# Performance work log

Measured on AMD Instinct MI355X. Metric: run time of the kernel, lower is better.

The kernel has to match this reference:

```python
import jax, jax.numpy as jnp
import numpy as np

N_NODES = 100000
IN_C, HID_C, OUT_C = 128, 64, 40
N_EDGES = 1600000


def setup_inputs() -> dict:
    key = jax.random.key(0)
    k1, k2, k3, k4, k5, k6 = jax.random.split(key, 6)
    x = jax.random.normal(k1, (N_NODES, IN_C), dtype=jnp.float32)
    edge_index = jax.random.randint(k2, (2, N_EDGES), 0, N_NODES, dtype=jnp.int32)
    # Glorot-style init for GCN weights, zero bias (as in PyG GCNConv)
    W1 = jax.random.normal(k3, (IN_C, HID_C), dtype=jnp.float32) / np.sqrt(IN_C)
    b1 = jnp.zeros((HID_C,), dtype=jnp.float32)
    W2 = jax.random.normal(k4, (HID_C, OUT_C), dtype=jnp.float32) / np.sqrt(HID_C)
    b2 = jnp.zeros((OUT_C,), dtype=jnp.float32)
    return {"x": x, "edge_index": edge_index, "W1": W1, "b1": b1, "W2": W2, "b2": b2}


def gcn_conv(x, src, dst, W, b, n_nodes):
    # PyG GCNConv: self-loops added, symmetric deg^{-1/2} normalization,
    # linear transform first, then normalized scatter-sum aggregation, then bias.
    deg = jnp.zeros((n_nodes,), dtype=x.dtype).at[dst].add(1.0)
    dinv = jnp.where(deg > 0, jax.lax.rsqrt(deg), 0.0)
    norm = dinv[src] * dinv[dst]                      # [E]
    h = x @ W                                          # [N, out]
    msg = h[src] * norm[:, None]                       # [E, out] (gather)
    out = jax.ops.segment_sum(msg, dst, num_segments=n_nodes)  # scatter-add
    return out + b


def reference(x, edge_index, W1, b1, W2, b2):
    n = x.shape[0]
    loop = jnp.arange(n, dtype=edge_index.dtype)
    src = jnp.concatenate([edge_index[0], loop])
    dst = jnp.concatenate([edge_index[1], loop])
    h = jax.nn.relu(gcn_conv(x, src, dst, W1, b1, n))
    # F.dropout with training=False -> identity (eval mode)
    return gcn_conv(h, src, dst, W2, b2, n)
```

## Files before the change

### kernel.cpp

```cpp
#include <hip/hip_runtime.h>

#define N_NODES 100000
#define IN_C    128
#define HID_C   64
#define OUT_C   40
#define N_EDGES 1600000

#define BSH        8
#define NBUCK      ((N_NODES + 255) >> BSH)
#define CAP        5120
#define PART_CHUNK 4096
#define NPB        ((N_EDGES + PART_CHUNK - 1) / PART_CHUNK)
#define EPT        (PART_CHUNK / 256)

typedef _Float16 half_t;
typedef _Float16 half8   __attribute__((ext_vector_type(8)));
typedef _Float16 half2_t __attribute__((ext_vector_type(2)));
typedef float    f32x4   __attribute__((ext_vector_type(4)));
typedef unsigned long long ull;

static __device__ __forceinline__ void acc8(float* a, uint2 v, float sc) {
    char4 lo = __builtin_bit_cast(char4, v.x);
    char4 hi = __builtin_bit_cast(char4, v.y);
    a[0] += sc * (float)lo.x; a[1] += sc * (float)lo.y;
    a[2] += sc * (float)lo.z; a[3] += sc * (float)lo.w;
    a[4] += sc * (float)hi.x; a[5] += sc * (float)hi.y;
    a[6] += sc * (float)hi.z; a[7] += sc * (float)hi.w;
}

static __device__ __forceinline__ void acc_q(float4& a, unsigned v, float sc, bool ok) {
    char4 c = __builtin_bit_cast(char4, v);
    if (ok) {
        a.x += sc * (float)c.x;
        a.y += sc * (float)c.y;
        a.z += sc * (float)c.z;
        a.w += sc * (float)c.w;
    }
}

__global__ void k_init(const float* __restrict__ W1, const float* __restrict__ W2,
                       half_t* __restrict__ W1T, half_t* __restrict__ W2T,
                       int* __restrict__ gcur) {
    int t = threadIdx.x;
    if (t < NBUCK) gcur[t] = t * CAP;
    for (int i = t; i < IN_C * HID_C; i += 512) {
        int k = i >> 6, n = i & 63;
        W1T[n * IN_C + k] = (half_t)W1[i];
    }
    for (int i = t; i < 48 * HID_C; i += 512) {
        int n = i >> 6, k = i & 63;
        W2T[n * HID_C + k] = (n < OUT_C) ? (half_t)W2[k * OUT_C + n] : (half_t)0.0f;
    }
}

__global__ void k_part(const int* __restrict__ src, const int* __restrict__ dst,
                       int* __restrict__ gcur, ull* __restrict__ pairs) {
    __shared__ int lh[NBUCK];
    int tid = threadIdx.x;
    for (int i = tid; i < NBUCK; i += 256) lh[i] = 0;
    __syncthreads();
    int base = blockIdx.x * PART_CHUNK;
    int sv[EPT], dv[EPT], rv[EPT];
#pragma unroll
    for (int j = 0; j < EPT; ++j) {
        int e = base + j * 256 + tid;
        if (e < N_EDGES) {
            sv[j] = src[e];
            dv[j] = dst[e];
            rv[j] = atomicAdd(&lh[dv[j] >> BSH], 1);
        } else {
            dv[j] = -1;
        }
    }
    __syncthreads();
    for (int i = tid; i < NBUCK; i += 256) {
        int c = lh[i];
        if (c) lh[i] = atomicAdd(&gcur[i], c);
    }
    __syncthreads();
#pragma unroll
    for (int j = 0; j < EPT; ++j) {
        if (dv[j] >= 0) {
            int pos = lh[dv[j] >> BSH] + rv[j];
            pairs[pos] = ((ull)(unsigned)dv[j] << 32) | (unsigned)sv[j];
        }
    }
}

__global__ void k_bbuild(const ull* __restrict__ pairs, const int* __restrict__ gcur,
                         int* __restrict__ cursor, int* __restrict__ cnt,
                         float* __restrict__ dinv, int* __restrict__ esrc) {
    __shared__ int lc[256];
    __shared__ int ls[256];
    __shared__ int lcur[256];
    int b = blockIdx.x, tid = threadIdx.x;
    int nbase = b << BSH;
    int s0 = b * CAP, s1 = gcur[b];

    lc[tid] = 0;
    __syncthreads();
    for (int e = s0 + tid; e < s1; e += 256)
        atomicAdd(&lc[(int)(pairs[e] >> 32) - nbase], 1);
    __syncthreads();

    int v = lc[tid];
    ls[tid] = v;
    __syncthreads();
    for (int off = 1; off < 256; off <<= 1) {
        int t = (tid >= off) ? ls[tid - off] : 0;
        __syncthreads();
        ls[tid] += t;
        __syncthreads();
    }
    int excl = ls[tid] - v;
    int node = nbase + tid;
    int rowstart = s0 + excl;
    lcur[tid] = rowstart;
    if (node < N_NODES) {
        cursor[node] = rowstart;
        cnt[node]    = v;
        dinv[node]   = rsqrtf(1.0f + (float)v);
    }
    __syncthreads();

    for (int e = s0 + tid; e < s1; e += 256) {
        ull p = pairs[e];
        int d = (int)(p >> 32);
        int s = (int)(p & 0xffffffffu);
        int pos = atomicAdd(&lcur[d - nbase], 1);
        esrc[pos] = s;
    }
}

__global__ void k_gemm1_mfma(const float* __restrict__ x, const half_t* __restrict__ W1T,
                             const float* __restrict__ dinv, signed char* __restrict__ g1q,
                             float* __restrict__ scales) {
    __shared__ __align__(16) signed char lq[16 * HID_C];
    int lane = threadIdx.x & 63;
    int l16  = lane & 15;
    int lg   = lane >> 4;

    half8 bf[4][4];
#pragma unroll
    for (int ct = 0; ct < 4; ++ct)
#pragma unroll
        for (int kc = 0; kc < 4; ++kc)
            bf[ct][kc] = *(const half8*)(W1T + (ct * 16 + l16) * IN_C + kc * 32 + lg * 8);

#pragma unroll
    for (int s = 0; s < 2; ++s) {
        int r0 = (blockIdx.x * 2 + s) * 16;
        f32x4 acc0 = {0.f, 0.f, 0.f, 0.f};
        f32x4 acc1 = {0.f, 0.f, 0.f, 0.f};
        f32x4 acc2 = {0.f, 0.f, 0.f, 0.f};
        f32x4 acc3 = {0.f, 0.f, 0.f, 0.f};
#pragma unroll
        for (int kc = 0; kc < 4; ++kc) {
            const float* ap = x + (size_t)(r0 + l16) * IN_C + kc * 32 + lg * 8;
            float4 a0 = *(const float4*)ap;
            float4 a1 = *(const float4*)(ap + 4);
            half8 af;
            af[0] = (_Float16)a0.x; af[1] = (_Float16)a0.y;
            af[2] = (_Float16)a0.z; af[3] = (_Float16)a0.w;
            af[4] = (_Float16)a1.x; af[5] = (_Float16)a1.y;
            af[6] = (_Float16)a1.z; af[7] = (_Float16)a1.w;
            acc0 = __builtin_amdgcn_mfma_f32_16x16x32_f16(af, bf[0][kc], acc0, 0, 0, 0);
            acc1 = __builtin_amdgcn_mfma_f32_16x16x32_f16(af, bf[1][kc], acc1, 0, 0, 0);
            acc2 = __builtin_amdgcn_mfma_f32_16x16x32_f16(af, bf[2][kc], acc2, 0, 0, 0);
            acc3 = __builtin_amdgcn_mfma_f32_16x16x32_f16(af, bf[3][kc], acc3, 0, 0, 0);
        }
#pragma unroll
        for (int j = 0; j < 4; ++j) {
            int   r  = r0 + lg * 4 + j;
            float dv = dinv[r];
            float v0 = acc0[j] * dv;
            float v1 = acc1[j] * dv;
            float v2 = acc2[j] * dv;
            float v3 = acc3[j] * dv;
            float m = fmaxf(fmaxf(fabsf(v0), fabsf(v1)), fmaxf(fabsf(v2), fabsf(v3)));
            m = fmaxf(m, __shfl_xor(m, 1));
            m = fmaxf(m, __shfl_xor(m, 2));
            m = fmaxf(m, __shfl_xor(m, 4));
            m = fmaxf(m, __shfl_xor(m, 8));
            float inv = (m > 0.0f) ? 127.0f / m : 0.0f;
            if (l16 == 0) scales[r] = m * (1.0f / 127.0f);
            int q0 = min(127, max(-127, __float2int_rn(v0 * inv)));
            int q1 = min(127, max(-127, __float2int_rn(v1 * inv)));
            int q2 = min(127, max(-127, __float2int_rn(v2 * inv)));
            int q3 = min(127, max(-127, __float2int_rn(v3 * inv)));
            int rl = lg * 4 + j;
            lq[rl * HID_C +  0 + l16] = (signed char)q0;
            lq[rl * HID_C + 16 + l16] = (signed char)q1;
            lq[rl * HID_C + 32 + l16] = (signed char)q2;
            lq[rl * HID_C + 48 + l16] = (signed char)q3;
        }
        uint4 wv = *(const uint4*)(lq + lane * 16);
        *(uint4*)(g1q + (size_t)r0 * HID_C + lane * 16) = wv;
    }
}

__global__ void k_pull1(const int* __restrict__ cursor, const int* __restrict__ cnt,
                        const int* __restrict__ esrc, const float* __restrict__ dinv,
                        const uint2* __restrict__ g1v, const float* __restrict__ scales,
                        const float* __restrict__ b1, half_t* __restrict__ h1) {
    int w    = threadIdx.x >> 6;
    int lane = threadIdx.x & 63;
    int n    = blockIdx.x * 4 + w;
    int slot = lane >> 3;
    int c8   = lane & 7;

    float dn  = dinv[n];
    int start = cursor[n];
    int end   = start + cnt[n];

    float a[8] = {0.f, 0.f, 0.f, 0.f, 0.f, 0.f, 0.f, 0.f};
    if (slot == 0)
        acc8(a, g1v[(size_t)n * 8 + c8], scales[n]);

    int e = start;
    for (; e + 16 <= end; e += 16) {
        int i0 = esrc[e + slot];
        int i1 = esrc[e + 8 + slot];
        uint2 v0 = g1v[(size_t)i0 * 8 + c8];
        float s0 = scales[i0];
        uint2 v1 = g1v[(size_t)i1 * 8 + c8];
        float s1 = scales[i1];
        acc8(a, v0, s0);
        acc8(a, v1, s1);
    }
    for (; e < end; e += 8) {
        int  ee  = e + slot;
        bool ok  = ee < end;
        int  idx = esrc[ok ? ee : end - 1];
        uint2 v = g1v[(size_t)idx * 8 + c8];
        float s = ok ? scales[idx] : 0.f;
        acc8(a, v, s);
    }

#pragma unroll
    for (int j = 0; j < 8; ++j) {
        a[j] += __shfl_xor(a[j], 8);
        a[j] += __shfl_xor(a[j], 16);
        a[j] += __shfl_xor(a[j], 32);
    }

    if (slot == 0) {
        const float* bp = b1 + c8 * 8;
        float r0 = fmaxf(dn * a[0] + bp[0], 0.f);
        float r1 = fmaxf(dn * a[1] + bp[1], 0.f);
        float r2 = fmaxf(dn * a[2] + bp[2], 0.f);
        float r3 = fmaxf(dn * a[3] + bp[3], 0.f);
        float r4 = fmaxf(dn * a[4] + bp[4], 0.f);
        float r5 = fmaxf(dn * a[5] + bp[5], 0.f);
        float r6 = fmaxf(dn * a[6] + bp[6], 0.f);
        float r7 = fmaxf(dn * a[7] + bp[7], 0.f);
        half2_t p0; p0.x = (_Float16)r0; p0.y = (_Float16)r1;
        half2_t p1; p1.x = (_Float16)r2; p1.y = (_Float16)r3;
        half2_t p2; p2.x = (_Float16)r4; p2.y = (_Float16)r5;
        half2_t p3; p3.x = (_Float16)r6; p3.y = (_Float16)r7;
        uint4 u;
        u.x = __builtin_bit_cast(unsigned, p0);
        u.y = __builtin_bit_cast(unsigned, p1);
        u.z = __builtin_bit_cast(unsigned, p2);
        u.w = __builtin_bit_cast(unsigned, p3);
        *(uint4*)(h1 + (size_t)n * HID_C + c8 * 8) = u;
    }
}

__global__ void k_gemm2_mfma(const half_t* __restrict__ h1, const half_t* __restrict__ W2T,
                             const float* __restrict__ dinv, signed char* __restrict__ g2q,
                             float* __restrict__ scales2) {
    __shared__ __align__(16) signed char lq[16 * 40];
    int lane = threadIdx.x & 63;
    int l16  = lane & 15;
    int lg   = lane >> 4;

    half8 bf[3][2];
#pragma unroll
    for (int ct = 0; ct < 3; ++ct)
#pragma unroll
        for (int kc = 0; kc < 2; ++kc)
            bf[ct][kc] = *(const half8*)(W2T + (ct * 16 + l16) * HID_C + kc * 32 + lg * 8);

#pragma unroll
    for (int s = 0; s < 2; ++s) {
        int r0 = (blockIdx.x * 2 + s) * 16;
        f32x4 acc0 = {0.f, 0.f, 0.f, 0.f};
        f32x4 acc1 = {0.f, 0.f, 0.f, 0.f};
        f32x4 acc2 = {0.f, 0.f, 0.f, 0.f};
#pragma unroll
        for (int kc = 0; kc < 2; ++kc) {
            half8 af = *(const half8*)(h1 + (size_t)(r0 + l16) * HID_C + kc * 32 + lg * 8);
            acc0 = __builtin_amdgcn_mfma_f32_16x16x32_f16(af, bf[0][kc], acc0, 0, 0, 0);
            acc1 = __builtin_amdgcn_mfma_f32_16x16x32_f16(af, bf[1][kc], acc1, 0, 0, 0);
            acc2 = __builtin_amdgcn_mfma_f32_16x16x32_f16(af, bf[2][kc], acc2, 0, 0, 0);
        }
#pragma unroll
        for (int j = 0; j < 4; ++j) {
            int   r  = r0 + lg * 4 + j;
            float dv = dinv[r];
            float v0 = acc0[j] * dv;
            float v1 = acc1[j] * dv;
            float v2 = (l16 < 8) ? acc2[j] * dv : 0.0f;
            float m = fmaxf(fmaxf(fabsf(v0), fabsf(v1)), fabsf(v2));
            m = fmaxf(m, __shfl_xor(m, 1));
            m = fmaxf(m, __shfl_xor(m, 2));
            m = fmaxf(m, __shfl_xor(m, 4));
            m = fmaxf(m, __shfl_xor(m, 8));
            float inv = (m > 0.0f) ? 127.0f / m : 0.0f;
            if (l16 == 0) scales2[r] = m * (1.0f / 127.0f);
            int q0 = min(127, max(-127, __float2int_rn(v0 * inv)));
            int q1 = min(127, max(-127, __float2int_rn(v1 * inv)));
            int q2 = min(127, max(-127, __float2int_rn(v2 * inv)));
            int rl = lg * 4 + j;
            lq[rl * 40 +  0 + l16] = (signed char)q0;
            lq[rl * 40 + 16 + l16] = (signed char)q1;
            if (l16 < 8) lq[rl * 40 + 32 + l16] = (signed char)q2;
        }
        if (lane < 40)
            *(uint4*)(g2q + (size_t)r0 * 40 + lane * 16) = *(const uint4*)(lq + lane * 16);
    }
}

__global__ void k_pull2(const int* __restrict__ cursor, const int* __restrict__ cnt,
                        const int* __restrict__ esrc, const float* __restrict__ dinv,
                        const signed char* __restrict__ g2q, const float* __restrict__ scales2,
                        const float* __restrict__ b2, float* __restrict__ out) {
    int w    = threadIdx.x >> 6;
    int lane = threadIdx.x & 63;
    int n    = blockIdx.x * 4 + w;
    int slot = lane >> 3;
    int c8   = lane & 7;

    float dn  = dinv[n];
    int start = cursor[n];
    int end   = start + cnt[n];

    float a[8] = {0.f, 0.f, 0.f, 0.f, 0.f, 0.f, 0.f, 0.f};
    if (slot == 0) {
        uint2 v = *(const uint2*)(g2q + (size_t)n * 40 + c8 * 8);
        acc8(a, v, scales2[n]);
    }

    int e = start;
    for (; e + 16 <= end; e += 16) {
        int i0 = esrc[e + slot];
        int i1 = esrc[e + 8 + slot];
        uint2 v0 = *(const uint2*)(g2q + (size_t)i0 * 40 + c8 * 8);
        float s0 = scales2[i0];
        uint2 v1 = *(const uint2*)(g2q + (size_t)i1 * 40 + c8 * 8);
        float s1 = scales2[i1];
        acc8(a, v0, s0);
        acc8(a, v1, s1);
    }
    for (; e < end; e += 8) {
        int  ee  = e + slot;
        bool ok  = ee < end;
        int  idx = esrc[ok ? ee : end - 1];
        uint2 v = *(const uint2*)(g2q + (size_t)idx * 40 + c8 * 8);
        float s = ok ? scales2[idx] : 0.f;
        acc8(a, v, s);
    }

#pragma unroll
    for (int j = 0; j < 8; ++j) {
        a[j] += __shfl_xor(a[j], 8);
        a[j] += __shfl_xor(a[j], 16);
        a[j] += __shfl_xor(a[j], 32);
    }

    if (slot == 0 && c8 < 5) {
        const float* bp = b2 + c8 * 8;
        float* op = out + (size_t)n * OUT_C + c8 * 8;
        float4 r0, r1;
        r0.x = bp[0] + dn * a[0];
        r0.y = bp[1] + dn * a[1];
        r0.z = bp[2] + dn * a[2];
        r0.w = bp[3] + dn * a[3];
        r1.x = bp[4] + dn * a[4];
        r1.y = bp[5] + dn * a[5];
        r1.z = bp[6] + dn * a[6];
        r1.w = bp[7] + dn * a[7];
        *(float4*)op = r0;
        *(float4*)(op + 4) = r1;
    }
}

extern "C" void kernel_launch(void* const* d_in, const int* in_sizes, int n_in,
                              void* d_out, int out_size, void* d_ws, size_t ws_size,
                              hipStream_t stream) {
    const float* x   = (const float*)d_in[0];
    const int*   ei  = (const int*)d_in[1];
    const int*   src = ei;
    const int*   dst = ei + N_EDGES;
    const float* W1  = (const float*)d_in[2];
    const float* b1  = (const float*)d_in[3];
    const float* W2  = (const float*)d_in[4];
    const float* b2  = (const float*)d_in[5];
    float*       out = (float*)d_out;

    const int SLAB = NBUCK * CAP;
    int*    cnt    = (int*)d_ws;
    int*    cursor = cnt + N_NODES;
    int*    gcur   = cursor + N_NODES;
    half_t* w1t    = (half_t*)(gcur + NBUCK);
    half_t* w2t    = w1t + IN_C * HID_C;
    float*  dinv   = (float*)(w2t + 48 * HID_C);
    float*  scales = dinv + N_NODES;
    float*  scales2= scales + N_NODES;
    int*    esrc   = (int*)(scales2 + N_NODES);
    int*    after  = esrc + SLAB;
    ull*    pairs  = (ull*)(((uintptr_t)after + 15) & ~(uintptr_t)15);
    signed char* g1q = (signed char*)(pairs + SLAB);
    half_t* h1 = (half_t*)(g1q + (size_t)N_NODES * 64);
    signed char* g2q = (signed char*)(h1 + (size_t)N_NODES * HID_C);

    k_init<<<1, 512, 0, stream>>>(W1, W2, w1t, w2t, gcur);
    k_part<<<NPB, 256, 0, stream>>>(src, dst, gcur, pairs);
    k_bbuild<<<NBUCK, 256, 0, stream>>>(pairs, gcur, cursor, cnt, dinv, esrc);

    k_gemm1_mfma<<<N_NODES / 32, 64, 0, stream>>>(x, w1t, dinv, g1q, scales);

    k_pull1<<<N_NODES / 4, 256, 0, stream>>>(cursor, cnt, esrc, dinv,
                                             (const uint2*)g1q, scales, b1, h1);

    k_gemm2_mfma<<<N_NODES / 32, 64, 0, stream>>>(h1, w2t, dinv, g2q, scales2);

    k_pull2<<<N_NODES / 4, 256, 0, stream>>>(cursor, cnt, esrc, dinv,
                                             g2q, scales2, b2, out);
}
```

Baseline: 169.8 us.

## Split layer-1 quantized features into two column halves and aggregate each separately

```diff
diff --git a/kernel.cpp b/kernel.cpp
--- a/kernel.cpp
+++ b/kernel.cpp
@@ -133,7 +133,8 @@
 }
 
 __global__ void k_gemm1_mfma(const float* __restrict__ x, const half_t* __restrict__ W1T,
-                             const float* __restrict__ dinv, signed char* __restrict__ g1q,
+                             const float* __restrict__ dinv,
+                             signed char* __restrict__ g1qA, signed char* __restrict__ g1qB,
                              float* __restrict__ scales) {
     __shared__ __align__(16) signed char lq[16 * HID_C];
     int lane = threadIdx.x & 63;
@@ -194,76 +195,82 @@
             lq[rl * HID_C + 32 + l16] = (signed char)q2;
             lq[rl * HID_C + 48 + l16] = (signed char)q3;
         }
-        uint4 wv = *(const uint4*)(lq + lane * 16);
-        *(uint4*)(g1q + (size_t)r0 * HID_C + lane * 16) = wv;
-    }
-}
-
-__global__ void k_pull1(const int* __restrict__ cursor, const int* __restrict__ cnt,
-                        const int* __restrict__ esrc, const float* __restrict__ dinv,
-                        const uint2* __restrict__ g1v, const float* __restrict__ scales,
-                        const float* __restrict__ b1, half_t* __restrict__ h1) {
+        {
+            int row = lane >> 2;
+            int q   = lane & 3;
+            uint2 av = *(const uint2*)(lq + row * HID_C + q * 8);
+            uint2 bv = *(const uint2*)(lq + row * HID_C + 32 + q * 8);
+            *(uint2*)(g1qA + (size_t)(r0 + row) * 32 + q * 8) = av;
+            *(uint2*)(g1qB + (size_t)(r0 + row) * 32 + q * 8) = bv;
+        }
+    }
+}
+
+__global__ void k_pull1h(const int* __restrict__ cursor, const int* __restrict__ cnt,
+                         const int* __restrict__ esrc, const float* __restrict__ dinv,
+                         const unsigned* __restrict__ g1h, const float* __restrict__ scales,
+                         const float* __restrict__ b1h, half_t* __restrict__ h1h) {
     int w    = threadIdx.x >> 6;
     int lane = threadIdx.x & 63;
     int n    = blockIdx.x * 4 + w;
     int slot = lane >> 3;
-    int c8   = lane & 7;
+    int c4   = lane & 7;
 
     float dn  = dinv[n];
     int start = cursor[n];
     int end   = start + cnt[n];
 
-    float a[8] = {0.f, 0.f, 0.f, 0.f, 0.f, 0.f, 0.f, 0.f};
+    float4 acc = {0.f, 0.f, 0.f, 0.f};
     if (slot == 0)
-        acc8(a, g1v[(size_t)n * 8 + c8], scales[n]);
+        acc_q(acc, g1h[(size_t)n * 8 + c4], scales[n], true);
 
     int e = start;
-    for (; e + 16 <= end; e += 16) {
+    for (; e + 32 <= end; e += 32) {
         int i0 = esrc[e + slot];
         int i1 = esrc[e + 8 + slot];
-        uint2 v0 = g1v[(size_t)i0 * 8 + c8];
-        float s0 = scales[i0];
-        uint2 v1 = g1v[(size_t)i1 * 8 + c8];
-        float s1 = scales[i1];
-        acc8(a, v0, s0);
-        acc8(a, v1, s1);
+        int i2 = esrc[e + 16 + slot];
+        int i3 = esrc[e + 24 + slot];
+        unsigned v0 = g1h[(size_t)i0 * 8 + c4];
+        float    s0 = scales[i0];
+        unsigned v1 = g1h[(size_t)i1 * 8 + c4];
+        float    s1 = scales[i1];
+        unsigned v2 = g1h[(size_t)i2 * 8 + c4];
+        float    s2 = scales[i2];
+        unsigned v3 = g1h[(size_t)i3 * 8 + c4];
+        float    s3 = scales[i3];
+        acc_q(acc, v0, s0, true);
+        acc_q(acc, v1, s1, true);
+        acc_q(acc, v2, s2, true);
+        acc_q(acc, v3, s3, true);
     }
     for (; e < end; e += 8) {
         int  ee  = e + slot;
         bool ok  = ee < end;
         int  idx = esrc[ok ? ee : end - 1];
-        uint2 v = g1v[(size_t)idx * 8 + c8];
-        float s = ok ? scales[idx] : 0.f;
-        acc8(a, v, s);
-    }
-
-#pragma unroll
-    for (int j = 0; j < 8; ++j) {
-        a[j] += __shfl_xor(a[j], 8);
-        a[j] += __shfl_xor(a[j], 16);
-        a[j] += __shfl_xor(a[j], 32);
-    }
+        unsigned v = g1h[(size_t)idx * 8 + c4];
+        float    s = scales[idx];
+        acc_q(acc, v, s, ok);
+    }
+
+    acc.x += __shfl_xor(acc.x, 8);  acc.y += __shfl_xor(acc.y, 8);
+    acc.z += __shfl_xor(acc.z, 8);  acc.w += __shfl_xor(acc.w, 8);
+    acc.x += __shfl_xor(acc.x, 16); acc.y += __shfl_xor(acc.y, 16);
+    acc.z += __shfl_xor(acc.z, 16); acc.w += __shfl_xor(acc.w, 16);
+    acc.x += __shfl_xor(acc.x, 32); acc.y += __shfl_xor(acc.y, 32);
+    acc.z += __shfl_xor(acc.z, 32); acc.w += __shfl_xor(acc.w, 32);
 
     if (slot == 0) {
-        const float* bp = b1 + c8 * 8;
-        float r0 = fmaxf(dn * a[0] + bp[0], 0.f);
-        float r1 = fmaxf(dn * a[1] + bp[1], 0.f);
-        float r2 = fmaxf(dn * a[2] + bp[2], 0.f);
-        float r3 = fmaxf(dn * a[3] + bp[3], 0.f);
-        float r4 = fmaxf(dn * a[4] + bp[4], 0.f);
-        float r5 = fmaxf(dn * a[5] + bp[5], 0.f);
-        float r6 = fmaxf(dn * a[6] + bp[6], 0.f);
-        float r7 = fmaxf(dn * a[7] + bp[7], 0.f);
-        half2_t p0; p0.x = (_Float16)r0; p0.y = (_Float16)r1;
-        half2_t p1; p1.x = (_Float16)r2; p1.y = (_Float16)r3;
-        half2_t p2; p2.x = (_Float16)r4; p2.y = (_Float16)r5;
-        half2_t p3; p3.x = (_Float16)r6; p3.y = (_Float16)r7;
-        uint4 u;
+        float4 bb = ((const float4*)b1h)[c4];
+        float rx = fmaxf(dn * acc.x + bb.x, 0.0f);
+        float ry = fmaxf(dn * acc.y + bb.y, 0.0f);
+        float rz = fmaxf(dn * acc.z + bb.z, 0.0f);
+        float rw = fmaxf(dn * acc.w + bb.w, 0.0f);
+        half2_t p0; p0.x = (_Float16)rx; p0.y = (_Float16)ry;
+        half2_t p1; p1.x = (_Float16)rz; p1.y = (_Float16)rw;
+        uint2 u;
         u.x = __builtin_bit_cast(unsigned, p0);
         u.y = __builtin_bit_cast(unsigned, p1);
-        u.z = __builtin_bit_cast(unsigned, p2);
-        u.w = __builtin_bit_cast(unsigned, p3);
-        *(uint4*)(h1 + (size_t)n * HID_C + c8 * 8) = u;
+        *(uint2*)(h1h + (size_t)n * HID_C + c4 * 4) = u;
     }
 }
 
@@ -403,26 +410,29 @@
     int*    cnt    = (int*)d_ws;
     int*    cursor = cnt + N_NODES;
     int*    gcur   = cursor + N_NODES;
-    half_t* w1t    = (half_t*)(gcur + NBUCK);
+    half_t* w1t    = (half_t*)(gcur + 512);
     half_t* w2t    = w1t + IN_C * HID_C;
     float*  dinv   = (float*)(w2t + 48 * HID_C);
     float*  scales = dinv + N_NODES;
     float*  scales2= scales + N_NODES;
     int*    esrc   = (int*)(scales2 + N_NODES);
     int*    after  = esrc + SLAB;
-    ull*    pairs  = (ull*)(((uintptr_t)after + 15) & ~(uintptr_t)15);
-    signed char* g1q = (signed char*)(pairs + SLAB);
-    half_t* h1 = (half_t*)(g1q + (size_t)N_NODES * 64);
+    ull*    pairs  = (ull*)(((uintptr_t)after + 127) & ~(uintptr_t)127);
+    signed char* g1qA = (signed char*)(pairs + SLAB);
+    signed char* g1qB = g1qA + (size_t)N_NODES * 32;
+    half_t* h1 = (half_t*)(g1qB + (size_t)N_NODES * 32);
     signed char* g2q = (signed char*)(h1 + (size_t)N_NODES * HID_C);
 
     k_init<<<1, 512, 0, stream>>>(W1, W2, w1t, w2t, gcur);
     k_part<<<NPB, 256, 0, stream>>>(src, dst, gcur, pairs);
     k_bbuild<<<NBUCK, 256, 0, stream>>>(pairs, gcur, cursor, cnt, dinv, esrc);
 
-    k_gemm1_mfma<<<N_NODES / 32, 64, 0, stream>>>(x, w1t, dinv, g1q, scales);
-
-    k_pull1<<<N_NODES / 4, 256, 0, stream>>>(cursor, cnt, esrc, dinv,
-                                             (const uint2*)g1q, scales, b1, h1);
+    k_gemm1_mfma<<<N_NODES / 32, 64, 0, stream>>>(x, w1t, dinv, g1qA, g1qB, scales);
+
+    k_pull1h<<<N_NODES / 4, 256, 0, stream>>>(cursor, cnt, esrc, dinv,
+                                              (const unsigned*)g1qA, scales, b1, h1);
+    k_pull1h<<<N_NODES / 4, 256, 0, stream>>>(cursor, cnt, esrc, dinv,
+                                              (const unsigned*)g1qB, scales, b1 + 32, h1 + 32);
 
     k_gemm2_mfma<<<N_NODES / 32, 64, 0, stream>>>(h1, w2t, dinv, g2q, scales2);
 
```

Result: slower. 200.1 us (+17.9%).

## Split partition pairs into src array and byte dst, widen pull1 loads

Applied to the files above, without the earlier changes.

```diff
diff --git a/kernel.cpp b/kernel.cpp
--- a/kernel.cpp
+++ b/kernel.cpp
@@ -28,14 +28,19 @@
     a[6] += sc * (float)hi.z; a[7] += sc * (float)hi.w;
 }
 
-static __device__ __forceinline__ void acc_q(float4& a, unsigned v, float sc, bool ok) {
-    char4 c = __builtin_bit_cast(char4, v);
-    if (ok) {
-        a.x += sc * (float)c.x;
-        a.y += sc * (float)c.y;
-        a.z += sc * (float)c.z;
-        a.w += sc * (float)c.w;
-    }
+static __device__ __forceinline__ void acc16(float* a, uint4 v, float sc) {
+    char4 c0 = __builtin_bit_cast(char4, v.x);
+    char4 c1 = __builtin_bit_cast(char4, v.y);
+    char4 c2 = __builtin_bit_cast(char4, v.z);
+    char4 c3 = __builtin_bit_cast(char4, v.w);
+    a[0]  += sc * (float)c0.x; a[1]  += sc * (float)c0.y;
+    a[2]  += sc * (float)c0.z; a[3]  += sc * (float)c0.w;
+    a[4]  += sc * (float)c1.x; a[5]  += sc * (float)c1.y;
+    a[6]  += sc * (float)c1.z; a[7]  += sc * (float)c1.w;
+    a[8]  += sc * (float)c2.x; a[9]  += sc * (float)c2.y;
+    a[10] += sc * (float)c2.z; a[11] += sc * (float)c2.w;
+    a[12] += sc * (float)c3.x; a[13] += sc * (float)c3.y;
+    a[14] += sc * (float)c3.z; a[15] += sc * (float)c3.w;
 }
 
 __global__ void k_init(const float* __restrict__ W1, const float* __restrict__ W2,
@@ -54,7 +59,8 @@
 }
 
 __global__ void k_part(const int* __restrict__ src, const int* __restrict__ dst,
-                       int* __restrict__ gcur, ull* __restrict__ pairs) {
+                       int* __restrict__ gcur, int* __restrict__ srcs,
+                       unsigned char* __restrict__ d8) {
     __shared__ int lh[NBUCK];
     int tid = threadIdx.x;
     for (int i = tid; i < NBUCK; i += 256) lh[i] = 0;
@@ -82,14 +88,16 @@
     for (int j = 0; j < EPT; ++j) {
         if (dv[j] >= 0) {
             int pos = lh[dv[j] >> BSH] + rv[j];
-            pairs[pos] = ((ull)(unsigned)dv[j] << 32) | (unsigned)sv[j];
-        }
-    }
-}
-
-__global__ void k_bbuild(const ull* __restrict__ pairs, const int* __restrict__ gcur,
-                         int* __restrict__ cursor, int* __restrict__ cnt,
-                         float* __restrict__ dinv, int* __restrict__ esrc) {
+            srcs[pos] = sv[j];
+            d8[pos]   = (unsigned char)(dv[j] & 255);
+        }
+    }
+}
+
+__global__ void k_bbuild(const int* __restrict__ srcs, const unsigned char* __restrict__ d8,
+                         const int* __restrict__ gcur, int* __restrict__ cursor,
+                         int* __restrict__ cnt, float* __restrict__ dinv,
+                         int* __restrict__ esrc) {
     __shared__ int lc[256];
     __shared__ int ls[256];
     __shared__ int lcur[256];
@@ -100,7 +108,7 @@
     lc[tid] = 0;
     __syncthreads();
     for (int e = s0 + tid; e < s1; e += 256)
-        atomicAdd(&lc[(int)(pairs[e] >> 32) - nbase], 1);
+        atomicAdd(&lc[d8[e]], 1);
     __syncthreads();
 
     int v = lc[tid];
@@ -124,10 +132,9 @@
     __syncthreads();
 
     for (int e = s0 + tid; e < s1; e += 256) {
-        ull p = pairs[e];
-        int d = (int)(p >> 32);
-        int s = (int)(p & 0xffffffffu);
-        int pos = atomicAdd(&lcur[d - nbase], 1);
+        int d = d8[e];
+        int s = srcs[e];
+        int pos = atomicAdd(&lcur[d], 1);
         esrc[pos] = s;
     }
 }
@@ -201,69 +208,80 @@
 
 __global__ void k_pull1(const int* __restrict__ cursor, const int* __restrict__ cnt,
                         const int* __restrict__ esrc, const float* __restrict__ dinv,
-                        const uint2* __restrict__ g1v, const float* __restrict__ scales,
+                        const uint4* __restrict__ g1v, const float* __restrict__ scales,
                         const float* __restrict__ b1, half_t* __restrict__ h1) {
     int w    = threadIdx.x >> 6;
     int lane = threadIdx.x & 63;
-    int n    = blockIdx.x * 4 + w;
-    int slot = lane >> 3;
-    int c8   = lane & 7;
+    int hl   = lane & 31;
+    int hh   = lane >> 5;
+    int slot = hl >> 2;
+    int c16  = hl & 3;
+    int n    = blockIdx.x * 8 + w * 2 + hh;
 
     float dn  = dinv[n];
     int start = cursor[n];
-    int end   = start + cnt[n];
-
-    float a[8] = {0.f, 0.f, 0.f, 0.f, 0.f, 0.f, 0.f, 0.f};
+    int mycnt = cnt[n];
+
+    float a[16];
+#pragma unroll
+    for (int j = 0; j < 16; ++j) a[j] = 0.f;
     if (slot == 0)
-        acc8(a, g1v[(size_t)n * 8 + c8], scales[n]);
-
-    int e = start;
-    for (; e + 16 <= end; e += 16) {
-        int i0 = esrc[e + slot];
-        int i1 = esrc[e + 8 + slot];
-        uint2 v0 = g1v[(size_t)i0 * 8 + c8];
-        float s0 = scales[i0];
-        uint2 v1 = g1v[(size_t)i1 * 8 + c8];
-        float s1 = scales[i1];
-        acc8(a, v0, s0);
-        acc8(a, v1, s1);
-    }
-    for (; e < end; e += 8) {
-        int  ee  = e + slot;
-        bool ok  = ee < end;
-        int  idx = esrc[ok ? ee : end - 1];
-        uint2 v = g1v[(size_t)idx * 8 + c8];
+        acc16(a, g1v[(size_t)n * 4 + c16], scales[n]);
+
+    int maxcnt = max(mycnt, __shfl_xor(mycnt, 32));
+
+    int e = 0;
+    for (; e + 16 <= maxcnt; e += 16) {
+        bool ok0 = (e + slot) < mycnt;
+        bool ok1 = (e + 8 + slot) < mycnt;
+        int i0 = esrc[ok0 ? (start + e + slot) : start];
+        int i1 = esrc[ok1 ? (start + e + 8 + slot) : start];
+        i0 = ok0 ? i0 : 0;
+        i1 = ok1 ? i1 : 0;
+        uint4 v0 = g1v[(size_t)i0 * 4 + c16];
+        float s0 = ok0 ? scales[i0] : 0.f;
+        uint4 v1 = g1v[(size_t)i1 * 4 + c16];
+        float s1 = ok1 ? scales[i1] : 0.f;
+        acc16(a, v0, s0);
+        acc16(a, v1, s1);
+    }
+    for (; e < maxcnt; e += 8) {
+        bool ok = (e + slot) < mycnt;
+        int idx = esrc[ok ? (start + e + slot) : start];
+        idx = ok ? idx : 0;
+        uint4 v = g1v[(size_t)idx * 4 + c16];
         float s = ok ? scales[idx] : 0.f;
-        acc8(a, v, s);
-    }
-
-#pragma unroll
-    for (int j = 0; j < 8; ++j) {
+        acc16(a, v, s);
+    }
+
+#pragma unroll
+    for (int j = 0; j < 16; ++j) {
+        a[j] += __shfl_xor(a[j], 4);
         a[j] += __shfl_xor(a[j], 8);
         a[j] += __shfl_xor(a[j], 16);
-        a[j] += __shfl_xor(a[j], 32);
     }
 
     if (slot == 0) {
-        const float* bp = b1 + c8 * 8;
-        float r0 = fmaxf(dn * a[0] + bp[0], 0.f);
-        float r1 = fmaxf(dn * a[1] + bp[1], 0.f);
-        float r2 = fmaxf(dn * a[2] + bp[2], 0.f);
-        float r3 = fmaxf(dn * a[3] + bp[3], 0.f);
-        float r4 = fmaxf(dn * a[4] + bp[4], 0.f);
-        float r5 = fmaxf(dn * a[5] + bp[5], 0.f);
-        float r6 = fmaxf(dn * a[6] + bp[6], 0.f);
-        float r7 = fmaxf(dn * a[7] + bp[7], 0.f);
-        half2_t p0; p0.x = (_Float16)r0; p0.y = (_Float16)r1;
-        half2_t p1; p1.x = (_Float16)r2; p1.y = (_Float16)r3;
-        half2_t p2; p2.x = (_Float16)r4; p2.y = (_Float16)r5;
-        half2_t p3; p3.x = (_Float16)r6; p3.y = (_Float16)r7;
-        uint4 u;
-        u.x = __builtin_bit_cast(unsigned, p0);
-        u.y = __builtin_bit_cast(unsigned, p1);
-        u.z = __builtin_bit_cast(unsigned, p2);
-        u.w = __builtin_bit_cast(unsigned, p3);
-        *(uint4*)(h1 + (size_t)n * HID_C + c8 * 8) = u;
+        const float4* bp = (const float4*)(b1 + c16 * 16);
+        uint4 u0, u1;
+        unsigned us[8];
+#pragma unroll
+        for (int q = 0; q < 4; ++q) {
+            float4 bb = bp[q];
+            float r0 = fmaxf(dn * a[q * 4 + 0] + bb.x, 0.f);
+            float r1 = fmaxf(dn * a[q * 4 + 1] + bb.y, 0.f);
+            float r2 = fmaxf(dn * a[q * 4 + 2] + bb.z, 0.f);
+            float r3 = fmaxf(dn * a[q * 4 + 3] + bb.w, 0.f);
+            half2_t p0; p0.x = (_Float16)r0; p0.y = (_Float16)r1;
+            half2_t p1; p1.x = (_Float16)r2; p1.y = (_Float16)r3;
+            us[q * 2 + 0] = __builtin_bit_cast(unsigned, p0);
+            us[q * 2 + 1] = __builtin_bit_cast(unsigned, p1);
+        }
+        u0.x = us[0]; u0.y = us[1]; u0.z = us[2]; u0.w = us[3];
+        u1.x = us[4]; u1.y = us[5]; u1.z = us[6]; u1.w = us[7];
+        half_t* hp = h1 + (size_t)n * HID_C + c16 * 16;
+        *(uint4*)hp = u0;
+        *(uint4*)(hp + 8) = u1;
     }
 }
 
@@ -403,26 +421,26 @@
     int*    cnt    = (int*)d_ws;
     int*    cursor = cnt + N_NODES;
     int*    gcur   = cursor + N_NODES;
-    half_t* w1t    = (half_t*)(gcur + NBUCK);
+    half_t* w1t    = (half_t*)(gcur + 512);
     half_t* w2t    = w1t + IN_C * HID_C;
     float*  dinv   = (float*)(w2t + 48 * HID_C);
     float*  scales = dinv + N_NODES;
     float*  scales2= scales + N_NODES;
-    int*    esrc   = (int*)(scales2 + N_NODES);
-    int*    after  = esrc + SLAB;
-    ull*    pairs  = (ull*)(((uintptr_t)after + 15) & ~(uintptr_t)15);
-    signed char* g1q = (signed char*)(pairs + SLAB);
+    int*    srcs   = (int*)(scales2 + N_NODES);
+    int*    esrc   = srcs + SLAB + 8;
+    unsigned char* d8 = (unsigned char*)(esrc + SLAB + 8);
+    signed char* g1q = (signed char*)(((uintptr_t)(d8 + SLAB) + 127) & ~(uintptr_t)127);
     half_t* h1 = (half_t*)(g1q + (size_t)N_NODES * 64);
     signed char* g2q = (signed char*)(h1 + (size_t)N_NODES * HID_C);
 
     k_init<<<1, 512, 0, stream>>>(W1, W2, w1t, w2t, gcur);
-    k_part<<<NPB, 256, 0, stream>>>(src, dst, gcur, pairs);
-    k_bbuild<<<NBUCK, 256, 0, stream>>>(pairs, gcur, cursor, cnt, dinv, esrc);
+    k_part<<<NPB, 256, 0, stream>>>(src, dst, gcur, srcs, d8);
+    k_bbuild<<<NBUCK, 256, 0, stream>>>(srcs, d8, gcur, cursor, cnt, dinv, esrc);
 
     k_gemm1_mfma<<<N_NODES / 32, 64, 0, stream>>>(x, w1t, dinv, g1q, scales);
 
-    k_pull1<<<N_NODES / 4, 256, 0, stream>>>(cursor, cnt, esrc, dinv,
-                                             (const uint2*)g1q, scales, b1, h1);
+    k_pull1<<<N_NODES / 8, 256, 0, stream>>>(cursor, cnt, esrc, dinv,
+                                             (const uint4*)g1q, scales, b1, h1);
 
     k_gemm2_mfma<<<N_NODES / 32, 64, 0, stream>>>(h1, w2t, dinv, g2q, scales2);
 
```

New measurement: 164.2 us. 3.3% less time.
